# Kernel tuning notes

Hardware: AMD Instinct MI355X
Metric: run time of the kernel (lower is better)

## Reference

```python
import jax, jax.numpy as jnp
import numpy as np

N_SUBJECTS = 64
N_LABELS = 16
DENS_TEMP = 0.1  # args.ProtoSim_dens_temp


def setup_inputs() -> dict:
    key = jax.random.key(0)
    k1, k2, k3 = jax.random.split(key, 3)
    B, V, D = 16384, 2, 512
    X_data = jax.random.normal(k1, (B, V, D), dtype=jnp.float32)
    subject = jax.random.randint(k2, (B,), 0, N_SUBJECTS)
    labels = jax.random.randint(k3, (B,), 0, N_LABELS)
    return {"X_data": X_data, "subject": subject, "labels": labels}


def reference(X_data, subject, labels):
    B, V, D = X_data.shape  # V == contrast_count == 2 (code doubles subject/labels once)
    K = N_SUBJECTS * N_LABELS
    # torch.cat(torch.unbind(X, dim=1), dim=0) -> [V*B, D]
    cf = jnp.transpose(X_data, (1, 0, 2)).reshape(V * B, D)
    subj2 = jnp.concatenate([subject, subject])
    lab2 = jnp.concatenate([labels, labels])
    # group id: groups enumerated sorted-by-(subject,label), i.e. g = s*C + l
    gid = subj2 * N_LABELS + lab2
    ones = jnp.ones((V * B,), dtype=cf.dtype)
    counts = jax.ops.segment_sum(ones, gid, num_segments=K)  # [K]
    safe_cnt = jnp.maximum(counts, 1.0)
    centroid = jax.ops.segment_sum(cf, gid, num_segments=K) / safe_cnt[:, None]  # [K, D]
    # per-sample euclidean distance to own group centroid (torch.cdist)
    dist = jnp.linalg.norm(cf - centroid[gid], axis=1)  # [V*B]
    # density_g = mean(sqrt(dist)) / log(n_g + 10) for n_g > 1, else dmax; then clip & scale
    mean_sqrt = jax.ops.segment_sum(jnp.sqrt(dist), gid, num_segments=K) / safe_cnt
    density = mean_sqrt / jnp.log(counts + 10.0)
    density = jnp.where(counts > 1, density, 0.0)
    density = jnp.where(counts > 1, density, density.max())
    density = jnp.clip(density, jnp.percentile(density, 10), jnp.percentile(density, 90))
    density = DENS_TEMP * density / density.mean()
    density = jax.lax.stop_gradient(density)  # torch builds it via .tolist()/numpy
    # mask: different subject AND same label vs each group prototype
    g_subj = jnp.arange(K) // N_LABELS
    g_lab = jnp.arange(K) % N_LABELS
    mask = ((subj2[:, None] != g_subj[None, :]) & (lab2[:, None] == g_lab[None, :])).astype(cf.dtype)  # [V*B, K]
    # with N_SUBJECTS > 1 every row has >= 1 positive group -> no rows deleted
    sim = jnp.matmul(cf, centroid.T) / density[None, :]  # [V*B, K]
    sim = sim - jax.lax.stop_gradient(jnp.max(sim, axis=1, keepdims=True))
    positive_sim = sim * mask
    # CrossEntropyLoss(reduction='none') with soft (unnormalized) targets = mask
    logp = jax.nn.log_softmax(positive_sim, axis=1)
    loss_per_row = -(mask * logp).sum(axis=1) / mask.sum(axis=1)
    return loss_per_row.mean()
```

## Files before the change

### kernel.cpp

```cpp
#include <hip/hip_runtime.h>


typedef __bf16 v8bf __attribute__((ext_vector_type(8)));
typedef __bf16 v4bf __attribute__((ext_vector_type(4)));
typedef float  v4f  __attribute__((ext_vector_type(4)));
typedef unsigned int u32x4 __attribute__((ext_vector_type(4)));

#define B_ROWS 16384
#define ROWS   32768
#define NGRP   1024
#define DIM    512
#define LOG2E  1.4426950408889634f
#define LN2    0.6931471805599453f

__device__ __forceinline__ float wredSum(float v){
#pragma unroll
  for (int o = 32; o > 0; o >>= 1) v += __shfl_xor(v, o);
  return v;
}
__device__ __forceinline__ float wredMax(float v){
#pragma unroll
  for (int o = 32; o > 0; o >>= 1) v = fmaxf(v, __shfl_xor(v, o));
  return v;
}

__global__ void kA2(const int* __restrict__ subj, const int* __restrict__ lab,
                    int* __restrict__ base_cnt, int* __restrict__ gid_arr){
  int i = blockIdx.x * 256 + threadIdx.x;
  int g = subj[i] * 16 + lab[i];
  gid_arr[i] = g;
  atomicAdd(&base_cnt[g], 1);
}

__global__ void kA3(const int* __restrict__ base_cnt, int* __restrict__ offs,
                    int* __restrict__ fillp){
  __shared__ int sb[NGRP];
  int t = threadIdx.x;
  int c = base_cnt[t];
  sb[t] = c;
  __syncthreads();
  for (int off = 1; off < NGRP; off <<= 1){
    int v = (t >= off) ? sb[t - off] : 0;
    __syncthreads();
    sb[t] += v;
    __syncthreads();
  }
  int ex = sb[t] - c;
  offs[t] = ex;
  fillp[t] = ex;
}

__global__ void kA4(const int* __restrict__ gid_arr, int* __restrict__ fillp,
                    int* __restrict__ row_list){
  int i = blockIdx.x * 256 + threadIdx.x;
  int pos = atomicAdd(&fillp[gid_arr[i]], 1);
  row_list[pos] = i;
}

__global__ void kB(const float* __restrict__ X, const int* __restrict__ base_cnt,
                   const int* __restrict__ offs, const int* __restrict__ row_list,
                   float* __restrict__ cent_f, __bf16* __restrict__ cent_b){
  int g = blockIdx.x, t = threadIdx.x;
  int n = base_cnt[g], off = offs[g];
  float ax = 0.f, ay = 0.f, az = 0.f, aw = 0.f;
  for (int j = 0; j < n; ++j){
    int r = row_list[off + j];
    const float4* p = (const float4*)(X + (size_t)r * 1024);
    float4 a = p[t];
    float4 b = p[t + 128];
    ax += a.x + b.x; ay += a.y + b.y; az += a.z + b.z; aw += a.w + b.w;
  }
  int cnt2 = 2 * n;
  float inv = 1.0f / (float)(cnt2 > 1 ? cnt2 : 1);
  float4 c; c.x = ax * inv; c.y = ay * inv; c.z = az * inv; c.w = aw * inv;
  ((float4*)(cent_f + (size_t)g * DIM))[t] = c;
  v4bf cb; cb[0] = (__bf16)c.x; cb[1] = (__bf16)c.y; cb[2] = (__bf16)c.z; cb[3] = (__bf16)c.w;
  *(v4bf*)(cent_b + (size_t)g * DIM + t * 4) = cb;
}

__global__ void kC(const float* __restrict__ X, const int* __restrict__ subj,
                   const int* __restrict__ lab, const float* __restrict__ cent_f,
                   float* __restrict__ msq, __bf16* __restrict__ cfb){
  int w = threadIdx.x >> 6, lane = threadIdx.x & 63;
  int r = blockIdx.x * 4 + w;
  int i = r & (B_ROWS - 1), v = r >> 14;
  int g = subj[i] * 16 + lab[i];
  const float4* xr = (const float4*)(X + ((size_t)(i * 2 + v)) * DIM);
  const float4* cr = (const float4*)(cent_f + (size_t)g * DIM);
  float4 x0 = xr[lane], x1 = xr[lane + 64];
  float4 c0 = cr[lane], c1 = cr[lane + 64];
  float s = 0.f, d;
  d = x0.x - c0.x; s += d * d;  d = x0.y - c0.y; s += d * d;
  d = x0.z - c0.z; s += d * d;  d = x0.w - c0.w; s += d * d;
  d = x1.x - c1.x; s += d * d;  d = x1.y - c1.y; s += d * d;
  d = x1.z - c1.z; s += d * d;  d = x1.w - c1.w; s += d * d;
  v4bf b0; b0[0]=(__bf16)x0.x; b0[1]=(__bf16)x0.y; b0[2]=(__bf16)x0.z; b0[3]=(__bf16)x0.w;
  v4bf b1; b1[0]=(__bf16)x1.x; b1[1]=(__bf16)x1.y; b1[2]=(__bf16)x1.z; b1[3]=(__bf16)x1.w;
  *(v4bf*)(cfb + (size_t)r * DIM + lane * 4)       = b0;
  *(v4bf*)(cfb + (size_t)r * DIM + 256 + lane * 4) = b1;
  s = wredSum(s);
  if (lane == 0){
    float dist = sqrtf(s);
    atomicAdd(&msq[g], sqrtf(dist));
  }
}

__global__ void kD(const int* __restrict__ base_cnt, const float* __restrict__ msq,
                   float* __restrict__ scale2){
  __shared__ float sd[NGRP];
  __shared__ float ss[NGRP];
  __shared__ float rb[16];
  int t = threadIdx.x;
  int lane = t & 63, wid = t >> 6;
  int cnt2 = 2 * base_cnt[t];
  float safe = (float)(cnt2 > 1 ? cnt2 : 1);
  float v = (msq[t] / safe) / logf((float)cnt2 + 10.0f);
  float d1 = (cnt2 > 1) ? v : 0.0f;
  float wm = wredMax(d1);
  if (lane == 0) rb[wid] = wm;
  __syncthreads();
  float x = (lane < 16) ? rb[lane] : -3.0e38f;
  if (wid == 0){ x = wredMax(x); if (lane == 0) rb[0] = x; }
  __syncthreads();
  float dmax = rb[0];
  float d2 = (cnt2 > 1) ? d1 : dmax;
  sd[t] = d2;
  __syncthreads();
  int rank = 0;
  for (int j = 0; j < NGRP; ++j){
    float dj = sd[j];
    rank += (dj < d2) || (dj == d2 && j < t);
  }
  ss[rank] = d2;
  __syncthreads();
  float p10 = ss[102] + 0.3f * (ss[103] - ss[102]);
  float p90 = ss[920] + 0.7f * (ss[921] - ss[920]);
  float c = fminf(fmaxf(d2, p10), p90);
  __syncthreads();
  float wsm = wredSum(c);
  if (lane == 0) rb[wid] = wsm;
  __syncthreads();
  float y = (lane < 16) ? rb[lane] : 0.0f;
  if (wid == 0){ y = wredSum(y); if (lane == 0) rb[0] = y; }
  __syncthreads();
  float mean = rb[0] * (1.0f / 1024.0f);
  scale2[t] = LOG2E * mean / (0.1f * c);
}

__global__ __launch_bounds__(256, 2)
void kE(const __bf16* __restrict__ cfb, const __bf16* __restrict__ centb,
        const float* __restrict__ scale2, const int* __restrict__ gid_arr,
        float* __restrict__ loss_sum){
  __shared__ u32x4 cent[2][128 * 9];
  __shared__ float sscale[NGRP];
  __shared__ float red[4];
  int tid = threadIdx.x, lane = tid & 63, w = tid >> 6;
  int l15 = lane & 15, lhi = lane >> 4;
  int row = blockIdx.x * 64 + w * 16 + l15;

  const u32x4* gA = (const u32x4*)centb;
  const u32x4* gB = (const u32x4*)cfb;

  ((v4f*)sscale)[tid] = ((const v4f*)scale2)[tid];

  u32x4 breg[16];
  {
    const u32x4* rp = gB + (size_t)row * 64 + lhi;
#pragma unroll
    for (int c = 0; c < 16; ++c) breg[c] = rp[c * 4];
  }

  int g = gid_arr[row & (B_ROWS - 1)];
  int rsub = g >> 4, rlab = g & 15;
  float labeq[4];
#pragma unroll
  for (int j = 0; j < 4; ++j) labeq[j] = (rlab == lhi * 4 + j) ? 1.0f : 0.0f;

  u32x4 st[4];
  auto stage = [&](int tt){
    int gb = tt >> 3, ks = tt & 7;
#pragma unroll
    for (int c2 = 0; c2 < 4; ++c2){
      int flat = c2 * 256 + tid;
      int mrow = flat >> 3, kidx = flat & 7;
      st[c2] = gA[(size_t)(gb * 128 + mrow) * 64 + ks * 8 + kidx];
    }
  };
  auto commit = [&](int buf){
#pragma unroll
    for (int c2 = 0; c2 < 4; ++c2){
      int flat = c2 * 256 + tid;
      int mrow = flat >> 3, kidx = flat & 7;
      cent[buf][mrow * 9 + kidx] = st[c2];
    }
  };

  v4f acc[8];
#pragma unroll
  for (int fm = 0; fm < 8; ++fm) acc[fm] = (v4f){0.f, 0.f, 0.f, 0.f};
  float M = -3.0e38f, E = 0.f, S = 0.f;

  stage(0); commit(0);
  __syncthreads();

  for (int gb = 0; gb < 8; ++gb){
#pragma unroll
    for (int ks = 0; ks < 8; ++ks){
      int tt = gb * 8 + ks;
      if (tt < 63) stage(tt + 1);
#pragma unroll
      for (int kk = 0; kk < 2; ++kk){
        v8bf afr[8];
#pragma unroll
        for (int fm = 0; fm < 8; ++fm){
          int mrow = fm * 16 + l15;
          afr[fm] = __builtin_bit_cast(v8bf, cent[ks & 1][mrow * 9 + kk * 4 + lhi]);
        }
#pragma unroll
        for (int fm = 0; fm < 8; ++fm)
          acc[fm] = __builtin_amdgcn_mfma_f32_16x16x32_bf16(
              afr[fm], __builtin_bit_cast(v8bf, breg[ks * 2 + kk]), acc[fm], 0, 0, 0);
      }
      if (tt < 63){
        commit((tt + 1) & 1);
        __syncthreads();
      }
    }
    {
      v4f vs[8];
      float mloc = -3.0e38f;
#pragma unroll
      for (int fm = 0; fm < 8; ++fm){
        v4f sc = *(const v4f*)&sscale[gb * 128 + fm * 16 + lhi * 4];
        v4f t;
#pragma unroll
        for (int j = 0; j < 4; ++j){
          t[j] = acc[fm][j] * sc[j];
          mloc = fmaxf(mloc, t[j]);
        }
        vs[fm] = t;
      }
      float Mn = fmaxf(M, mloc);
      float eadd = 0.f, sadd = 0.f;
#pragma unroll
      for (int fm = 0; fm < 8; ++fm){
        float subne = (rsub != gb * 8 + fm) ? 1.0f : 0.0f;
#pragma unroll
        for (int j = 0; j < 4; ++j){
          float mk = subne * labeq[j];
          eadd += mk * exp2f(vs[fm][j] - Mn);
          sadd += mk * vs[fm][j];
        }
      }
      E = E * exp2f(M - Mn) + eadd;
      S += sadd;
      M = Mn;
#pragma unroll
      for (int fm = 0; fm < 8; ++fm) acc[fm] = (v4f){0.f, 0.f, 0.f, 0.f};
    }
  }

#pragma unroll
  for (int off = 16; off < 64; off <<= 1){
    float mo = __shfl_xor(M, off);
    float eo = __shfl_xor(E, off);
    float so = __shfl_xor(S, off);
    float mn = fmaxf(M, mo);
    E = E * exp2f(M - mn) + eo * exp2f(mo - mn);
    S += so;
    M = mn;
  }
  float loss = logf(961.0f + E) + LN2 * M - LN2 * (S * (1.0f / 63.0f));
  float wsum = wredSum(loss) * 0.25f;
  if (lane == 0) red[w] = wsum;
  __syncthreads();
  if (tid == 0) atomicAdd(loss_sum, red[0] + red[1] + red[2] + red[3]);
}

__global__ void kG(const float* __restrict__ loss_sum, float* __restrict__ out){
  out[0] = loss_sum[0] * (1.0f / (float)ROWS);
}

extern "C" void kernel_launch(void* const* d_in, const int* in_sizes, int n_in,
                              void* d_out, int out_size, void* d_ws, size_t ws_size,
                              hipStream_t stream){
  const float* X   = (const float*)d_in[0];
  const int* subj  = (const int*)d_in[1];
  const int* lab   = (const int*)d_in[2];
  float* out = (float*)d_out;
  char* ws = (char*)d_ws;

  int*    base_cnt = (int*)(ws + 0);
  float*  msq      = (float*)(ws + 4096);
  float*  loss_s   = (float*)(ws + 8192);
  int*    offs     = (int*)(ws + 8448);
  int*    fillp    = (int*)(ws + 12544);
  int*    gid_arr  = (int*)(ws + 16640);
  int*    row_list = (int*)(ws + 82176);
  float*  scale2   = (float*)(ws + 147712);
  float*  cent_f   = (float*)(ws + 151808);
  __bf16* cent_b   = (__bf16*)(ws + 2248960);
  __bf16* cfb      = (__bf16*)(ws + 3297536);

  hipMemsetAsync(ws, 0, 8208, stream);

  kA2<<<64, 256, 0, stream>>>(subj, lab, base_cnt, gid_arr);
  kA3<<<1, 1024, 0, stream>>>(base_cnt, offs, fillp);
  kA4<<<64, 256, 0, stream>>>(gid_arr, fillp, row_list);
  kB <<<1024, 128, 0, stream>>>(X, base_cnt, offs, row_list, cent_f, cent_b);
  kC <<<8192, 256, 0, stream>>>(X, subj, lab, cent_f, msq, cfb);
  kD <<<1, 1024, 0, stream>>>(base_cnt, msq, scale2);
  kE <<<512, 256, 0, stream>>>(cfb, cent_b, scale2, gid_arr, loss_s);
  kG <<<1, 1, 0, stream>>>(loss_s, out);
}
```

Baseline: 166.8 us.

## Fuse preprocessing kernels and retile prototype GEMM with 32x32 MFMA and async LDS loads

Merges the three grouping kernels into one single-block kernel that uses LDS atomics. Fuses the centroid and distance kernels into a per-group kernel that reads each group's rows twice and writes bf16 features, which drops the fp32 centroid buffer and the global atomics. The loss GEMM is rebuilt with 512-thread blocks, 32x32x16 MFMA, XOR-swizzled LDS tiles filled by global_load_lds, and a cross-wave softmax merge that writes the scaled result straight to the output, removing the final kernel. The risks are a serial single-block grouping pass and load imbalance in the per-group kernel when group sizes differ.

```diff
diff --git a/kernel.cpp b/kernel.cpp
--- a/kernel.cpp
+++ b/kernel.cpp
@@ -4,12 +4,12 @@
 typedef __bf16 v8bf __attribute__((ext_vector_type(8)));
 typedef __bf16 v4bf __attribute__((ext_vector_type(4)));
 typedef float  v4f  __attribute__((ext_vector_type(4)));
+typedef float  v16f __attribute__((ext_vector_type(16)));
 typedef unsigned int u32x4 __attribute__((ext_vector_type(4)));
 
 #define B_ROWS 16384
 #define ROWS   32768
 #define NGRP   1024
-#define DIM    512
 #define LOG2E  1.4426950408889634f
 #define LN2    0.6931471805599453f
 
@@ -24,85 +24,108 @@
   return v;
 }
 
-__global__ void kA2(const int* __restrict__ subj, const int* __restrict__ lab,
-                    int* __restrict__ base_cnt, int* __restrict__ gid_arr){
-  int i = blockIdx.x * 256 + threadIdx.x;
-  int g = subj[i] * 16 + lab[i];
-  gid_arr[i] = g;
-  atomicAdd(&base_cnt[g], 1);
-}
-
-__global__ void kA3(const int* __restrict__ base_cnt, int* __restrict__ offs,
-                    int* __restrict__ fillp){
-  __shared__ int sb[NGRP];
+__device__ __forceinline__ void gload16(const void* g, void* lds){
+  __builtin_amdgcn_global_load_lds(
+      (const __attribute__((address_space(1))) void*)g,
+      (__attribute__((address_space(3))) void*)lds, 16, 0, 0);
+}
+
+__global__ __launch_bounds__(1024)
+void kA(const int* __restrict__ subj, const int* __restrict__ lab,
+        int* __restrict__ base_cnt, int* __restrict__ offs,
+        int* __restrict__ gid_arr, int* __restrict__ row_list){
+  __shared__ int cnt[NGRP];
+  __shared__ int fill[NGRP];
   int t = threadIdx.x;
-  int c = base_cnt[t];
-  sb[t] = c;
-  __syncthreads();
+  cnt[t] = 0;
+  __syncthreads();
+  int gl[16];
+#pragma unroll
+  for (int k = 0; k < 16; ++k){
+    int i = k * 1024 + t;
+    int g = subj[i] * 16 + lab[i];
+    gl[k] = g;
+    gid_arr[i] = g;
+    atomicAdd(&cnt[g], 1);
+  }
+  __syncthreads();
+  int c = cnt[t];
   for (int off = 1; off < NGRP; off <<= 1){
-    int v = (t >= off) ? sb[t - off] : 0;
+    int v = (t >= off) ? cnt[t - off] : 0;
     __syncthreads();
-    sb[t] += v;
+    cnt[t] += v;
     __syncthreads();
   }
-  int ex = sb[t] - c;
+  int ex = cnt[t] - c;
+  base_cnt[t] = c;
   offs[t] = ex;
-  fillp[t] = ex;
-}
-
-__global__ void kA4(const int* __restrict__ gid_arr, int* __restrict__ fillp,
-                    int* __restrict__ row_list){
-  int i = blockIdx.x * 256 + threadIdx.x;
-  int pos = atomicAdd(&fillp[gid_arr[i]], 1);
-  row_list[pos] = i;
-}
-
-__global__ void kB(const float* __restrict__ X, const int* __restrict__ base_cnt,
-                   const int* __restrict__ offs, const int* __restrict__ row_list,
-                   float* __restrict__ cent_f, __bf16* __restrict__ cent_b){
-  int g = blockIdx.x, t = threadIdx.x;
+  fill[t] = ex;
+  __syncthreads();
+#pragma unroll
+  for (int k = 0; k < 16; ++k){
+    int i = k * 1024 + t;
+    int pos = atomicAdd(&fill[gl[k]], 1);
+    row_list[pos] = i;
+  }
+}
+
+__global__ __launch_bounds__(128)
+void kBC(const float* __restrict__ X, const int* __restrict__ base_cnt,
+         const int* __restrict__ offs, const int* __restrict__ row_list,
+         __bf16* __restrict__ cent_b, float* __restrict__ msq,
+         __bf16* __restrict__ cfb){
+  __shared__ v4f cl[2][128];
+  __shared__ float mred[2];
+  int g = blockIdx.x;
+  int t = threadIdx.x, w = t >> 6, lane = t & 63;
   int n = base_cnt[g], off = offs[g];
-  float ax = 0.f, ay = 0.f, az = 0.f, aw = 0.f;
-  for (int j = 0; j < n; ++j){
+  v4f a0 = {0,0,0,0}, a1 = {0,0,0,0};
+  for (int j = w; j < n; j += 2){
     int r = row_list[off + j];
-    const float4* p = (const float4*)(X + (size_t)r * 1024);
-    float4 a = p[t];
-    float4 b = p[t + 128];
-    ax += a.x + b.x; ay += a.y + b.y; az += a.z + b.z; aw += a.w + b.w;
-  }
+    const v4f* p = (const v4f*)(X + (size_t)r * 1024);
+    a0 += p[lane] + p[lane + 128];
+    a1 += p[lane + 64] + p[lane + 192];
+  }
+  cl[w][lane] = a0; cl[w][lane + 64] = a1;
+  __syncthreads();
   int cnt2 = 2 * n;
   float inv = 1.0f / (float)(cnt2 > 1 ? cnt2 : 1);
-  float4 c; c.x = ax * inv; c.y = ay * inv; c.z = az * inv; c.w = aw * inv;
-  ((float4*)(cent_f + (size_t)g * DIM))[t] = c;
-  v4bf cb; cb[0] = (__bf16)c.x; cb[1] = (__bf16)c.y; cb[2] = (__bf16)c.z; cb[3] = (__bf16)c.w;
-  *(v4bf*)(cent_b + (size_t)g * DIM + t * 4) = cb;
-}
-
-__global__ void kC(const float* __restrict__ X, const int* __restrict__ subj,
-                   const int* __restrict__ lab, const float* __restrict__ cent_f,
-                   float* __restrict__ msq, __bf16* __restrict__ cfb){
-  int w = threadIdx.x >> 6, lane = threadIdx.x & 63;
-  int r = blockIdx.x * 4 + w;
-  int i = r & (B_ROWS - 1), v = r >> 14;
-  int g = subj[i] * 16 + lab[i];
-  const float4* xr = (const float4*)(X + ((size_t)(i * 2 + v)) * DIM);
-  const float4* cr = (const float4*)(cent_f + (size_t)g * DIM);
-  float4 x0 = xr[lane], x1 = xr[lane + 64];
-  float4 c0 = cr[lane], c1 = cr[lane + 64];
-  float s = 0.f, d;
-  d = x0.x - c0.x; s += d * d;  d = x0.y - c0.y; s += d * d;
-  d = x0.z - c0.z; s += d * d;  d = x0.w - c0.w; s += d * d;
-  d = x1.x - c1.x; s += d * d;  d = x1.y - c1.y; s += d * d;
-  d = x1.z - c1.z; s += d * d;  d = x1.w - c1.w; s += d * d;
-  v4bf b0; b0[0]=(__bf16)x0.x; b0[1]=(__bf16)x0.y; b0[2]=(__bf16)x0.z; b0[3]=(__bf16)x0.w;
-  v4bf b1; b1[0]=(__bf16)x1.x; b1[1]=(__bf16)x1.y; b1[2]=(__bf16)x1.z; b1[3]=(__bf16)x1.w;
-  *(v4bf*)(cfb + (size_t)r * DIM + lane * 4)       = b0;
-  *(v4bf*)(cfb + (size_t)r * DIM + 256 + lane * 4) = b1;
-  s = wredSum(s);
-  if (lane == 0){
-    float dist = sqrtf(s);
-    atomicAdd(&msq[g], sqrtf(dist));
-  }
+  v4f c0 = (cl[0][lane] + cl[1][lane]) * inv;
+  v4f c1 = (cl[0][lane + 64] + cl[1][lane + 64]) * inv;
+  if (w == 0){
+    v4bf b0, b1;
+#pragma unroll
+    for (int j = 0; j < 4; ++j){ b0[j] = (__bf16)c0[j]; b1[j] = (__bf16)c1[j]; }
+    *(v4bf*)(cent_b + (size_t)g * 512 + lane * 4)       = b0;
+    *(v4bf*)(cent_b + (size_t)g * 512 + 256 + lane * 4) = b1;
+  }
+  float am = 0.f;
+  for (int j = w; j < n; j += 2){
+    int r = row_list[off + j];
+    const v4f* p = (const v4f*)(X + (size_t)r * 1024);
+    v4f x0 = p[lane], x1 = p[lane + 64], x2 = p[lane + 128], x3 = p[lane + 192];
+    v4f e0 = x0 - c0, e1 = x1 - c1, e2 = x2 - c0, e3 = x3 - c1;
+    float s0 = e0[0]*e0[0]+e0[1]*e0[1]+e0[2]*e0[2]+e0[3]*e0[3]
+             + e1[0]*e1[0]+e1[1]*e1[1]+e1[2]*e1[2]+e1[3]*e1[3];
+    float s1 = e2[0]*e2[0]+e2[1]*e2[1]+e2[2]*e2[2]+e2[3]*e2[3]
+             + e3[0]*e3[0]+e3[1]*e3[1]+e3[2]*e3[2]+e3[3]*e3[3];
+    v4bf b0, b1, b2, b3;
+#pragma unroll
+    for (int q = 0; q < 4; ++q){
+      b0[q] = (__bf16)x0[q]; b1[q] = (__bf16)x1[q];
+      b2[q] = (__bf16)x2[q]; b3[q] = (__bf16)x3[q];
+    }
+    __bf16* r0 = cfb + (size_t)r * 512;
+    __bf16* r1 = cfb + (size_t)(B_ROWS + r) * 512;
+    *(v4bf*)(r0 + lane * 4) = b0;  *(v4bf*)(r0 + 256 + lane * 4) = b1;
+    *(v4bf*)(r1 + lane * 4) = b2;  *(v4bf*)(r1 + 256 + lane * 4) = b3;
+    s0 = wredSum(s0);
+    s1 = wredSum(s1);
+    if (lane == 0) am += sqrtf(sqrtf(s0)) + sqrtf(sqrtf(s1));
+  }
+  if (lane == 0) mred[w] = am;
+  __syncthreads();
+  if (t == 0) msq[g] = mred[0] + mred[1];
 }
 
 __global__ void kD(const int* __restrict__ base_cnt, const float* __restrict__ msq,
@@ -147,138 +170,132 @@
   scale2[t] = LOG2E * mean / (0.1f * c);
 }
 
-__global__ __launch_bounds__(256, 2)
+__global__ __launch_bounds__(512, 2)
 void kE(const __bf16* __restrict__ cfb, const __bf16* __restrict__ centb,
         const float* __restrict__ scale2, const int* __restrict__ gid_arr,
-        float* __restrict__ loss_sum){
-  __shared__ u32x4 cent[2][128 * 9];
+        float* __restrict__ out){
+  __shared__ u32x4 tile[2][2048];
   __shared__ float sscale[NGRP];
-  __shared__ float red[4];
-  int tid = threadIdx.x, lane = tid & 63, w = tid >> 6;
-  int l15 = lane & 15, lhi = lane >> 4;
-  int row = blockIdx.x * 64 + w * 16 + l15;
-
-  const u32x4* gA = (const u32x4*)centb;
-  const u32x4* gB = (const u32x4*)cfb;
-
-  ((v4f*)sscale)[tid] = ((const v4f*)scale2)[tid];
-
-  u32x4 breg[16];
+  __shared__ float redM[256], redE[256], redS[256];
+  int tid = threadIdx.x, lane = tid & 63;
+  int w = tid >> 6, h = w >> 2;
+  int l31 = lane & 31, lhi = lane >> 5;
+  int row = blockIdx.x * 128 + (w & 3) * 32 + l31;
+
+  if (tid < 256) ((v4f*)sscale)[tid] = ((const v4f*)scale2)[tid];
+
+  u32x4 breg[32];
   {
-    const u32x4* rp = gB + (size_t)row * 64 + lhi;
-#pragma unroll
-    for (int c = 0; c < 16; ++c) breg[c] = rp[c * 4];
-  }
-
-  int g = gid_arr[row & (B_ROWS - 1)];
-  int rsub = g >> 4, rlab = g & 15;
-  float labeq[4];
-#pragma unroll
-  for (int j = 0; j < 4; ++j) labeq[j] = (rlab == lhi * 4 + j) ? 1.0f : 0.0f;
-
-  u32x4 st[4];
-  auto stage = [&](int tt){
-    int gb = tt >> 3, ks = tt & 7;
-#pragma unroll
-    for (int c2 = 0; c2 < 4; ++c2){
-      int flat = c2 * 256 + tid;
-      int mrow = flat >> 3, kidx = flat & 7;
-      st[c2] = gA[(size_t)(gb * 128 + mrow) * 64 + ks * 8 + kidx];
+    const u32x4* rp = (const u32x4*)cfb + (size_t)row * 64 + lhi;
+#pragma unroll
+    for (int m = 0; m < 32; ++m) breg[m] = rp[2 * m];
+  }
+  int g0 = gid_arr[row & (B_ROWS - 1)];
+  int rsub = g0 >> 4, rlab = g0 & 15;
+
+  const char* gsrc = (const char*)centb;
+  auto stage = [&](int t2, int buf){
+    int i2 = t2 >> 3, ks2 = t2 & 7;
+#pragma unroll
+    for (int it = 0; it < 4; ++it){
+      int p = it * 512 + tid;
+      int trow = p >> 3, clin = p & 7;
+      int c = clin ^ (trow & 7);
+      int grow = i2 * 128 + (trow & 127) + ((trow >> 7) << 9);
+      const void* src = gsrc + ((size_t)(grow * 64 + ks2 * 8 + c) << 4);
+      void* dst = (void*)&tile[buf][it * 512 + (w << 6)];
+      gload16(src, dst);
     }
   };
-  auto commit = [&](int buf){
-#pragma unroll
-    for (int c2 = 0; c2 < 4; ++c2){
-      int flat = c2 * 256 + tid;
-      int mrow = flat >> 3, kidx = flat & 7;
-      cent[buf][mrow * 9 + kidx] = st[c2];
-    }
-  };
-
-  v4f acc[8];
-#pragma unroll
-  for (int fm = 0; fm < 8; ++fm) acc[fm] = (v4f){0.f, 0.f, 0.f, 0.f};
+
   float M = -3.0e38f, E = 0.f, S = 0.f;
-
-  stage(0); commit(0);
-  __syncthreads();
-
-  for (int gb = 0; gb < 8; ++gb){
-#pragma unroll
+  stage(0, 0);
+  __syncthreads();
+
+  for (int i = 0; i < 4; ++i){
+    v16f acc[4];
+#pragma unroll
+    for (int fm = 0; fm < 4; ++fm)
+#pragma unroll
+      for (int e = 0; e < 16; ++e) acc[fm][e] = 0.f;
+
     for (int ks = 0; ks < 8; ++ks){
-      int tt = gb * 8 + ks;
-      if (tt < 63) stage(tt + 1);
-#pragma unroll
-      for (int kk = 0; kk < 2; ++kk){
-        v8bf afr[8];
-#pragma unroll
-        for (int fm = 0; fm < 8; ++fm){
-          int mrow = fm * 16 + l15;
-          afr[fm] = __builtin_bit_cast(v8bf, cent[ks & 1][mrow * 9 + kk * 4 + lhi]);
-        }
-#pragma unroll
-        for (int fm = 0; fm < 8; ++fm)
-          acc[fm] = __builtin_amdgcn_mfma_f32_16x16x32_bf16(
-              afr[fm], __builtin_bit_cast(v8bf, breg[ks * 2 + kk]), acc[fm], 0, 0, 0);
-      }
-      if (tt < 63){
-        commit((tt + 1) & 1);
-        __syncthreads();
-      }
-    }
-    {
-      v4f vs[8];
-      float mloc = -3.0e38f;
-#pragma unroll
-      for (int fm = 0; fm < 8; ++fm){
-        v4f sc = *(const v4f*)&sscale[gb * 128 + fm * 16 + lhi * 4];
-        v4f t;
-#pragma unroll
-        for (int j = 0; j < 4; ++j){
-          t[j] = acc[fm][j] * sc[j];
-          mloc = fmaxf(mloc, t[j]);
-        }
-        vs[fm] = t;
-      }
-      float Mn = fmaxf(M, mloc);
-      float eadd = 0.f, sadd = 0.f;
-#pragma unroll
-      for (int fm = 0; fm < 8; ++fm){
-        float subne = (rsub != gb * 8 + fm) ? 1.0f : 0.0f;
-#pragma unroll
-        for (int j = 0; j < 4; ++j){
-          float mk = subne * labeq[j];
-          eadd += mk * exp2f(vs[fm][j] - Mn);
-          sadd += mk * vs[fm][j];
+      int t2 = i * 8 + ks;
+      int buf = t2 & 1;
+      if (t2 < 31) stage(t2 + 1, buf ^ 1);
+#pragma unroll
+      for (int kk = 0; kk < 4; ++kk){
+#pragma unroll
+        for (int fm = 0; fm < 4; ++fm){
+          int tr = h * 128 + fm * 32 + l31;
+          u32x4 af = tile[buf][tr * 8 + ((kk * 2 + lhi) ^ (tr & 7))];
+          acc[fm] = __builtin_amdgcn_mfma_f32_32x32x16_bf16(
+              __builtin_bit_cast(v8bf, af),
+              __builtin_bit_cast(v8bf, breg[ks * 4 + kk]),
+              acc[fm], 0, 0, 0);
         }
       }
-      E = E * exp2f(M - Mn) + eadd;
-      S += sadd;
-      M = Mn;
-#pragma unroll
-      for (int fm = 0; fm < 8; ++fm) acc[fm] = (v4f){0.f, 0.f, 0.f, 0.f};
-    }
-  }
-
-#pragma unroll
-  for (int off = 16; off < 64; off <<= 1){
-    float mo = __shfl_xor(M, off);
-    float eo = __shfl_xor(E, off);
-    float so = __shfl_xor(S, off);
+      __syncthreads();
+    }
+
+    float mloc = -3.0e38f;
+#pragma unroll
+    for (int fm = 0; fm < 4; ++fm){
+      int sbase = h * 512 + i * 128 + fm * 32 + lhi * 4;
+#pragma unroll
+      for (int q = 0; q < 4; ++q){
+        v4f sc = *(const v4f*)&sscale[sbase + q * 8];
+#pragma unroll
+        for (int j = 0; j < 4; ++j)
+          mloc = fmaxf(mloc, acc[fm][q * 4 + j] * sc[j]);
+      }
+    }
+    float Mn = fmaxf(M, mloc);
+    float eadd = 0.f, sadd = 0.f;
+#pragma unroll
+    for (int fm = 0; fm < 4; ++fm){
+      int sbase = h * 512 + i * 128 + fm * 32 + lhi * 4;
+      int gs_base = h * 32 + i * 8 + fm * 2;
+#pragma unroll
+      for (int q = 0; q < 4; ++q){
+        v4f sc = *(const v4f*)&sscale[sbase + q * 8];
+        float subne = ((gs_base + (q >> 1)) != rsub) ? 1.0f : 0.0f;
+#pragma unroll
+        for (int j = 0; j < 4; ++j){
+          int glab = j + ((q & 1) << 3) + (lhi << 2);
+          float mk = (glab == rlab) ? subne : 0.0f;
+          float vv = acc[fm][q * 4 + j] * sc[j];
+          eadd += mk * exp2f(vv - Mn);
+          sadd += mk * vv;
+        }
+      }
+    }
+    E = E * exp2f(M - Mn) + eadd;
+    S += sadd;
+    M = Mn;
+  }
+
+  {
+    float mo = __shfl_xor(M, 32), eo = __shfl_xor(E, 32), so = __shfl_xor(S, 32);
     float mn = fmaxf(M, mo);
     E = E * exp2f(M - mn) + eo * exp2f(mo - mn);
-    S += so;
-    M = mn;
-  }
-  float loss = logf(961.0f + E) + LN2 * M - LN2 * (S * (1.0f / 63.0f));
-  float wsum = wredSum(loss) * 0.25f;
-  if (lane == 0) red[w] = wsum;
-  __syncthreads();
-  if (tid == 0) atomicAdd(loss_sum, red[0] + red[1] + red[2] + red[3]);
-}
-
-__global__ void kG(const float* __restrict__ loss_sum, float* __restrict__ out){
-  out[0] = loss_sum[0] * (1.0f / (float)ROWS);
+    S += so; M = mn;
+  }
+  if (lhi == 0){
+    redM[w * 32 + l31] = M; redE[w * 32 + l31] = E; redS[w * 32 + l31] = S;
+  }
+  __syncthreads();
+  if (tid < 128){
+    int ww = tid >> 5, rr = tid & 31;
+    float m0 = redM[ww * 32 + rr], e0 = redE[ww * 32 + rr], s0 = redS[ww * 32 + rr];
+    float m1 = redM[(ww + 4) * 32 + rr], e1 = redE[(ww + 4) * 32 + rr], s1 = redS[(ww + 4) * 32 + rr];
+    float mn = fmaxf(m0, m1);
+    float Ee = e0 * exp2f(m0 - mn) + e1 * exp2f(m1 - mn);
+    float Ss = s0 + s1;
+    float loss = logf(961.0f + Ee) + LN2 * mn - LN2 * (Ss * (1.0f / 63.0f));
+    float ws = wredSum(loss);
+    if ((tid & 63) == 0) atomicAdd(out, ws * (1.0f / (float)ROWS));
+  }
 }
 
 extern "C" void kernel_launch(void* const* d_in, const int* in_sizes, int n_in,
@@ -287,29 +304,21 @@
   const float* X   = (const float*)d_in[0];
   const int* subj  = (const int*)d_in[1];
   const int* lab   = (const int*)d_in[2];
-  float* out = (float*)d_out;
   char* ws = (char*)d_ws;
 
   int*    base_cnt = (int*)(ws + 0);
-  float*  msq      = (float*)(ws + 4096);
-  float*  loss_s   = (float*)(ws + 8192);
-  int*    offs     = (int*)(ws + 8448);
-  int*    fillp    = (int*)(ws + 12544);
-  int*    gid_arr  = (int*)(ws + 16640);
-  int*    row_list = (int*)(ws + 82176);
-  float*  scale2   = (float*)(ws + 147712);
-  float*  cent_f   = (float*)(ws + 151808);
-  __bf16* cent_b   = (__bf16*)(ws + 2248960);
-  __bf16* cfb      = (__bf16*)(ws + 3297536);
-
-  hipMemsetAsync(ws, 0, 8208, stream);
-
-  kA2<<<64, 256, 0, stream>>>(subj, lab, base_cnt, gid_arr);
-  kA3<<<1, 1024, 0, stream>>>(base_cnt, offs, fillp);
-  kA4<<<64, 256, 0, stream>>>(gid_arr, fillp, row_list);
-  kB <<<1024, 128, 0, stream>>>(X, base_cnt, offs, row_list, cent_f, cent_b);
-  kC <<<8192, 256, 0, stream>>>(X, subj, lab, cent_f, msq, cfb);
+  int*    offs     = (int*)(ws + 4096);
+  int*    gid_arr  = (int*)(ws + 8192);
+  int*    row_list = (int*)(ws + 73728);
+  float*  msq      = (float*)(ws + 139264);
+  float*  scale2   = (float*)(ws + 143360);
+  __bf16* cent_b   = (__bf16*)(ws + 147456);
+  __bf16* cfb      = (__bf16*)(ws + 1196032);
+
+  hipMemsetAsync(d_out, 0, sizeof(float), stream);
+
+  kA <<<1, 1024, 0, stream>>>(subj, lab, base_cnt, offs, gid_arr, row_list);
+  kBC<<<NGRP, 128, 0, stream>>>(X, base_cnt, offs, row_list, cent_b, msq, cfb);
   kD <<<1, 1024, 0, stream>>>(base_cnt, msq, scale2);
-  kE <<<512, 256, 0, stream>>>(cfb, cent_b, scale2, gid_arr, loss_s);
-  kG <<<1, 1, 0, stream>>>(loss_s, out);
-}
+  kE <<<256, 512, 0, stream>>>(cfb, cent_b, scale2, gid_arr, (float*)d_out);
+}
```

Result: slower. 188.9 us (+13.2%).
